# Kernel optimization log

Hardware: AMD Instinct MI355X
Metric: run time of the kernel (lower is better)

Reference implementation:

```python
import jax, jax.numpy as jnp
import numpy as np

# Config (matches init_kwargs)
B, S = 2, 2048            # 2 packed sequences of 2048 tokens (prefill)
HQ, HK, D = 32, 8, 128    # GQA: 32 query heads, 8 kv heads
G = HQ // HK              # group size 4
WINDOW = 1024             # sliding window
THETA = 10000.0


def setup_inputs() -> dict:
    key = jax.random.key(0)
    kq, kk, kv = jax.random.split(key, 3)
    n_tokens = B * S
    query = jax.random.normal(kq, (n_tokens, HQ * D), dtype=jnp.float32)
    key_t = jax.random.normal(kk, (n_tokens, HK * D), dtype=jnp.float32)
    value = jax.random.normal(kv, (n_tokens, HK * D), dtype=jnp.float32)
    # per-sequence positions restart at 0 for each packed sequence
    positions = jnp.tile(jnp.arange(S, dtype=jnp.int32), B)
    return {"query": query, "key": key_t, "value": value, "positions": positions}


def _rope(x, positions):
    # x: [B, S, H, D]; rotate-half (NeoX) RoPE
    half = D // 2
    inv_freq = 1.0 / (THETA ** (jnp.arange(0, half, dtype=jnp.float32) / half))
    ang = positions.astype(jnp.float32)[:, None] * inv_freq[None, :]   # [B*S, D/2]
    cos = jnp.cos(ang).reshape(B, S, 1, half)
    sin = jnp.sin(ang).reshape(B, S, 1, half)
    x1, x2 = x[..., :half], x[..., half:]
    return jnp.concatenate([x1 * cos - x2 * sin, x2 * cos + x1 * sin], axis=-1)


def reference(query, key, value, positions):
    q = query.reshape(B, S, HQ, D)
    k = key.reshape(B, S, HK, D)
    v = value.reshape(B, S, HK, D)
    q = _rope(q, positions)
    k = _rope(k, positions)
    # GQA: split q heads into [HK, G]
    qg = q.reshape(B, S, HK, G, D)
    scale = 1.0 / jnp.sqrt(jnp.float32(D))
    # scores: [B, HK, G, Sq, Skv]
    scores = jnp.einsum('bqhgd,bshd->bhgqs', qg, k) * scale
    i = jnp.arange(S)[:, None]
    j = jnp.arange(S)[None, :]
    # causal + sliding window: j <= i and i - j < WINDOW
    mask = (j <= i) & ((i - j) < WINDOW)
    scores = jnp.where(mask[None, None, None], scores, jnp.float32(-1e30))
    attn = jax.nn.softmax(scores, axis=-1)
    out = jnp.einsum('bhgqs,bshd->bqhgd', attn, v)   # [B, Sq, HK, G, D]
    return out.reshape(B * S, HQ * D)
```

## Files before the change

### kernel.cpp

```cpp
#include <hip/hip_runtime.h>
#include <stdint.h>

#define NB 2
#define NS 2048
#define NHK 8
#define ND 128
#define NWIN 1024

using bf16x8 = __bf16 __attribute__((ext_vector_type(8)));
using f32x4  = float  __attribute__((ext_vector_type(4)));
using f32x2  = float  __attribute__((ext_vector_type(2)));
using f32x8  = float  __attribute__((ext_vector_type(8)));
using u16x8  = unsigned short __attribute__((ext_vector_type(8)));
using u32x4  = unsigned int   __attribute__((ext_vector_type(4)));

#define L2_10K (13.287712379549449f / 64.0f)
#define MASKV (-3.0e38f)

static __device__ __forceinline__ float ex2(float x) {
  return __builtin_amdgcn_exp2f(x);
}

static __device__ __forceinline__ unsigned short f2bf(float x) {
  unsigned int u = __builtin_bit_cast(unsigned int, x);
  u += 0x7FFFu + ((u >> 16) & 1u);
  return (unsigned short)(u >> 16);
}

static __device__ __forceinline__ unsigned int cvtpk(float lo, float hi) {
  unsigned int r;
  asm("v_cvt_pk_bf16_f32 %0, %1, %2" : "=v"(r) : "v"(lo), "v"(hi));
  return r;
}

static __device__ __forceinline__ void gll16(const void* g, void* l) {
  __builtin_amdgcn_global_load_lds(
      (const __attribute__((address_space(1))) void*)g,
      (__attribute__((address_space(3))) void*)l, 16, 0, 0);
}

__global__ __launch_bounds__(64) void build_tab(float* __restrict__ tab) {
  const int p = blockIdx.x, f = threadIdx.x;
  float s, c;
  __sincosf((float)p * ex2(-(float)f * L2_10K), &s, &c);
  tab[(size_t)p * 128 + f] = c;
  tab[(size_t)p * 128 + 64 + f] = s;
}

__global__ __launch_bounds__(256) void prepass(
    const float* __restrict__ kin, const float* __restrict__ vin,
    const int* __restrict__ pos, const float* __restrict__ tab,
    unsigned short* __restrict__ kimg, unsigned short* __restrict__ vimg) {
  const int bid = blockIdx.x;
  const int ti = bid & 63, gidx = bid >> 6;
  const int hk = gidx & 7, b = gidx >> 3;
  const int t = threadIdx.x;

  unsigned short* kout = kimg + (size_t)bid * 4096;
#pragma unroll
  for (int uu = 0; uu < 2; ++uu) {
    const int u = t * 2 + uu;
    const int j = u >> 4;
    const int d0 = ((u & 15) << 3) ^ ((j & 7) << 3);
    const int tok = (b << 11) + (ti << 5) + j;
    const float* kp = kin + (size_t)tok * (NHK * ND) + hk * ND;
    f32x8 a = *(const f32x8*)(kp + d0);
    f32x8 p = *(const f32x8*)(kp + (d0 ^ 64));
    const float* tr = tab + (size_t)(pos[tok] & 2047) * 128 + (d0 & 63);
    f32x8 c8 = *(const f32x8*)tr;
    f32x8 s8 = *(const f32x8*)(tr + 64);
    u16x8 o;
#pragma unroll
    for (int i = 0; i < 8; ++i) {
      float val = (d0 < 64) ? (a[i] * c8[i] - p[i] * s8[i])
                            : (a[i] * c8[i] + p[i] * s8[i]);
      o[i] = f2bf(val);
    }
    *(u16x8*)(kout + (size_t)u * 8) = o;
  }

  unsigned short* vout = vimg + (size_t)bid * 4096;
  {
    const int d0 = (t >> 2) << 1;
    const int kp4 = t & 3;
    const int tok0 = (b << 11) + (ti << 5) + (kp4 << 3);
    const float* vp = vin + (size_t)tok0 * (NHK * ND) + hk * ND + d0;
    u16x8 lo, hi;
#pragma unroll
    for (int i = 0; i < 8; ++i) {
      f32x2 r = *(const f32x2*)(vp + (size_t)i * (NHK * ND));
      lo[i] = f2bf(r[0]);
      hi[i] = f2bf(r[1]);
    }
    const int sub = kp4 ^ ((d0 >> 1) & 3);
    *(u16x8*)(vout + d0 * 32 + sub * 8) = lo;
    *(u16x8*)(vout + (d0 + 1) * 32 + sub * 8) = hi;
  }
}

template <bool PRE>
__global__ __launch_bounds__(256, 3) void attn_fwd(
    const float* __restrict__ qin, const float* __restrict__ kin,
    const float* __restrict__ vin, const int* __restrict__ pos,
    const char* __restrict__ kimg, const char* __restrict__ vimg,
    float* __restrict__ out) {
  __shared__ __align__(16) char Kb[2][8192];
  __shared__ __align__(16) char Vb[2][8192];

  const int B = blockIdx.x;
  const int group = (B & 7) + ((B >> 9) << 3);
  const int qt = 63 - ((B >> 3) & 63);
  const int hk = group & 7, b = group >> 3;

  const int tid = threadIdx.x;
  const int w = tid >> 6, lane = tid & 63, h = lane >> 4, ln = lane & 15;
  const int g = w;
  const int q0b = qt << 5;
  int lo = q0b - (NWIN - 1);
  if (lo < 0) lo = 0;
  lo &= ~31;
  const int ti0 = lo >> 5;
  const int nt = (q0b >> 5) - ti0 + 1;

  const size_t gbase = (size_t)group * 64 * 8192;
  const char* kg = PRE ? kimg + gbase + (size_t)(w * 128 + lane) * 16 : nullptr;
  const char* vg = PRE ? vimg + gbase + (size_t)(w * 128 + lane) * 16 : nullptr;

  auto stage = [&](int cur, int ti) {
    if constexpr (PRE) {
      const char* ks = kg + (size_t)ti * 8192;
      const char* vs = vg + (size_t)ti * 8192;
      char* kd = &Kb[cur][w * 2048];
      char* vd = &Vb[cur][w * 2048];
      gll16(ks, kd);
      gll16(ks + 1024, kd + 1024);
      gll16(vs, vd);
      gll16(vs + 1024, vd + 1024);
    } else {
      const int j = tid >> 3;
      const int du = (tid & 7) << 4;
      const int tok = (b << 11) + (ti << 5) + j;
      const float* kp = kin + (size_t)tok * (NHK * ND) + hk * ND;
      const float pj = (float)pos[tok];
#pragma unroll
      for (int gq = 0; gq < 2; ++gq) {
        const int dd = du + gq * 8;
        f32x8 a = *(const f32x8*)(kp + dd);
        f32x8 p = *(const f32x8*)(kp + (dd ^ 64));
        u16x8 o;
#pragma unroll
        for (int i = 0; i < 8; ++i) {
          float s, c;
          __sincosf(pj * ex2(-(float)((dd & 63) + i) * L2_10K), &s, &c);
          float val = (dd < 64) ? (a[i] * c - p[i] * s) : (a[i] * c + p[i] * s);
          o[i] = f2bf(val);
        }
        *(u16x8*)(&Kb[cur][((j << 8) + (dd << 1)) ^ ((j & 7) << 4)]) = o;
      }
      const int d0 = (tid >> 2) << 1;
      const int kp4 = tid & 3;
      const float* vp = vin + (size_t)((b << 11) + (ti << 5) + (kp4 << 3)) * (NHK * ND) + hk * ND + d0;
      u16x8 lov, hiv;
#pragma unroll
      for (int i = 0; i < 8; ++i) {
        f32x2 r = *(const f32x2*)(vp + (size_t)i * (NHK * ND));
        lov[i] = f2bf(r[0]);
        hiv[i] = f2bf(r[1]);
      }
      const int sub = kp4 ^ ((d0 >> 1) & 3);
      unsigned short* vb16 = (unsigned short*)Vb[cur];
      *(u16x8*)(vb16 + d0 * 32 + sub * 8) = lov;
      *(u16x8*)(vb16 + (d0 + 1) * 32 + sub * 8) = hiv;
    }
  };

  stage(0, ti0);

  const float QSC = 0.08838834764831845f * 1.4426950408889634f;
  bf16x8 qfr[2][4];
#pragma unroll
  for (int hf = 0; hf < 2; ++hf) {
    const int qrow = q0b + hf * 16 + ln;
    const size_t tokq = (size_t)(b << 11) + qrow;
    const float* qp = qin + tokq * 4096 + (hk * 4 + g) * 128;
    const float posq = (float)pos[tokq];
    const int r0 = h << 3;
    const int r1 = 32 + (h << 3);
    f32x8 a0 = *(const f32x8*)(qp + r0);
    f32x8 a1 = *(const f32x8*)(qp + r1);
    f32x8 a2 = *(const f32x8*)(qp + r0 + 64);
    f32x8 a3 = *(const f32x8*)(qp + r1 + 64);
    u16x8 u0, u1, u2, u3;
#pragma unroll
    for (int i = 0; i < 8; ++i) {
      float c0, s0, c1, s1;
      __sincosf(posq * ex2(-(float)(r0 + i) * L2_10K), &s0, &c0);
      __sincosf(posq * ex2(-(float)(r1 + i) * L2_10K), &s1, &c1);
      u0[i] = f2bf((a0[i] * c0 - a2[i] * s0) * QSC);
      u1[i] = f2bf((a1[i] * c1 - a3[i] * s1) * QSC);
      u2[i] = f2bf((a2[i] * c0 + a0[i] * s0) * QSC);
      u3[i] = f2bf((a3[i] * c1 + a1[i] * s1) * QSC);
    }
    qfr[hf][0] = __builtin_bit_cast(bf16x8, u0);
    qfr[hf][1] = __builtin_bit_cast(bf16x8, u1);
    qfr[hf][2] = __builtin_bit_cast(bf16x8, u2);
    qfr[hf][3] = __builtin_bit_cast(bf16x8, u3);
  }

  f32x4 Oc[2][8] = {};
  float msh[2] = {-1e30f, -1e30f};
  float lsum[2] = {};
  const int sw = (ln & 7) << 4;
  const int vsub = (h ^ ((ln >> 1) & 3)) << 4;

  for (int t = 0; t < nt; ++t) {
    const int cur = t & 1;
    asm volatile("s_waitcnt vmcnt(0)" ::: "memory");
    __syncthreads();
    if (t + 1 < nt) stage(cur ^ 1, ti0 + t + 1);

    const int j0 = (ti0 + t) << 5;
    const char* KB = Kb[cur];

    f32x4 sT[2][2] = {};
    __builtin_amdgcn_s_setprio(1);
#pragma unroll
    for (int c = 0; c < 4; ++c) {
      const bf16x8 k0 = *(const bf16x8*)(
          KB + (((ln << 8) + (c << 6) + (h << 4)) ^ sw));
      const bf16x8 k1 = *(const bf16x8*)(
          KB + ((((16 + ln) << 8) + (c << 6) + (h << 4)) ^ sw));
      sT[0][0] = __builtin_amdgcn_mfma_f32_16x16x32_bf16(k0, qfr[0][c], sT[0][0], 0, 0, 0);
      sT[0][1] = __builtin_amdgcn_mfma_f32_16x16x32_bf16(k1, qfr[0][c], sT[0][1], 0, 0, 0);
      sT[1][0] = __builtin_amdgcn_mfma_f32_16x16x32_bf16(k0, qfr[1][c], sT[1][0], 0, 0, 0);
      sT[1][1] = __builtin_amdgcn_mfma_f32_16x16x32_bf16(k1, qfr[1][c], sT[1][1], 0, 0, 0);
    }
    __builtin_amdgcn_s_setprio(0);

    if ((j0 >= q0b) || (j0 < q0b - 992)) {
#pragma unroll
      for (int qh = 0; qh < 2; ++qh) {
        const int irow = q0b + qh * 16 + ln;
#pragma unroll
        for (int ki = 0; ki < 2; ++ki)
#pragma unroll
          for (int r = 0; r < 4; ++r) {
            const int j = j0 + ki * 16 + (h << 2) + r;
            if (!(j <= irow && irow - j < NWIN)) sT[qh][ki][r] = MASKV;
          }
      }
    }

    float pm[2];
#pragma unroll
    for (int qh = 0; qh < 2; ++qh) {
      const f32x4 s0 = sT[qh][0], s1 = sT[qh][1];
      pm[qh] = fmaxf(fmaxf(fmaxf(s0[0], s0[1]), fmaxf(s0[2], s0[3])),
                     fmaxf(fmaxf(s1[0], s1[1]), fmaxf(s1[2], s1[3])));
    }
    const float ov = fmaxf(pm[0] - msh[0], pm[1] - msh[1]);
    if (__any(ov > 8.0f)) {
#pragma unroll
      for (int qh = 0; qh < 2; ++qh) {
        float M = pm[qh];
        M = fmaxf(M, __shfl_xor(M, 16));
        M = fmaxf(M, __shfl_xor(M, 32));
        const float mn = fmaxf(msh[qh], M);
        const float co = ex2(msh[qh] - mn);
        msh[qh] = mn;
        lsum[qh] *= co;
        float coO[4];
#pragma unroll
        for (int r = 0; r < 4; ++r) coO[r] = __shfl(co, (h << 2) + r);
#pragma unroll
        for (int db = 0; db < 8; ++db)
#pragma unroll
          for (int r = 0; r < 4; ++r) Oc[qh][db][r] *= coO[r];
      }
    }

    bf16x8 pa[2];
#pragma unroll
    for (int qh = 0; qh < 2; ++qh) {
      float e[2][4];
#pragma unroll
      for (int ki = 0; ki < 2; ++ki)
#pragma unroll
        for (int r = 0; r < 4; ++r) e[ki][r] = ex2(sT[qh][ki][r] - msh[qh]);
      lsum[qh] += ((e[0][0] + e[0][1]) + (e[0][2] + e[0][3])) +
                  ((e[1][0] + e[1][1]) + (e[1][2] + e[1][3]));
      unsigned int A = cvtpk(e[0][0], e[0][1]);
      unsigned int Bk = cvtpk(e[0][2], e[0][3]);
      unsigned int C = cvtpk(e[1][0], e[1][1]);
      unsigned int D = cvtpk(e[1][2], e[1][3]);
      asm volatile("v_permlane32_swap_b32 %0, %1" : "+v"(A), "+v"(C));
      asm volatile("v_permlane16_swap_b32 %0, %1" : "+v"(A), "+v"(C));
      asm volatile("v_permlane32_swap_b32 %0, %1" : "+v"(Bk), "+v"(D));
      asm volatile("v_permlane16_swap_b32 %0, %1" : "+v"(Bk), "+v"(D));
      u32x4 pk4 = {A, Bk, C, D};
      pa[qh] = __builtin_bit_cast(bf16x8, pk4);
    }

    const char* VB = Vb[cur];
    __builtin_amdgcn_s_setprio(1);
#pragma unroll
    for (int db = 0; db < 8; ++db) {
      const bf16x8 vv = *(const bf16x8*)(VB + (db << 10) + (ln << 6) + vsub);
      Oc[0][db] = __builtin_amdgcn_mfma_f32_16x16x32_bf16(pa[0], vv, Oc[0][db], 0, 0, 0);
      Oc[1][db] = __builtin_amdgcn_mfma_f32_16x16x32_bf16(pa[1], vv, Oc[1][db], 0, 0, 0);
    }
    __builtin_amdgcn_s_setprio(0);
  }

#pragma unroll
  for (int qh = 0; qh < 2; ++qh) {
    float ls = lsum[qh];
    ls += __shfl_xor(ls, 16);
    ls += __shfl_xor(ls, 32);
#pragma unroll
    for (int r = 0; r < 4; ++r) {
      const float rl = 1.0f / __shfl(ls, (h << 2) + r);
      const int irow = q0b + qh * 16 + (h << 2) + r;
      float* op = out + ((size_t)(b << 11) + irow) * 4096 + (hk * 4 + g) * 128 + ln;
#pragma unroll
      for (int db = 0; db < 8; ++db) op[db * 16] = Oc[qh][db][r] * rl;
    }
  }
}

extern "C" void kernel_launch(void* const* d_in, const int* in_sizes, int n_in,
                              void* d_out, int out_size, void* d_ws, size_t ws_size,
                              hipStream_t stream) {
  const float* q = (const float*)d_in[0];
  const float* k = (const float*)d_in[1];
  const float* v = (const float*)d_in[2];
  const int* pos = (const int*)d_in[3];
  float* out = (float*)d_out;

  const size_t TAB = (size_t)2048 * 128 * 4;
  const size_t KIMG = (size_t)16 * 64 * 8192;
  const size_t need = TAB + 2 * KIMG;

  if (ws_size >= need) {
    float* tab = (float*)d_ws;
    char* kimg = (char*)d_ws + TAB;
    char* vimg = kimg + KIMG;
    build_tab<<<2048, 64, 0, stream>>>(tab);
    prepass<<<1024, 256, 0, stream>>>(k, v, pos, tab,
                                      (unsigned short*)kimg, (unsigned short*)vimg);
    attn_fwd<true><<<1024, 256, 0, stream>>>(q, k, v, pos, kimg, vimg, out);
  } else {
    attn_fwd<false><<<1024, 256, 0, stream>>>(q, k, v, pos, nullptr, nullptr, out);
  }
}
```

Baseline: 94.15 us.

## Software-pipeline PV MFMA one tile behind QK and use RoPE table for Q

Result: no change. 95.23 us (+1.2%).

```diff
diff --git a/kernel.cpp b/kernel.cpp
--- a/kernel.cpp
+++ b/kernel.cpp
@@ -38,6 +38,11 @@
       (const __attribute__((address_space(1))) void*)g,
       (__attribute__((address_space(3))) void*)l, 16, 0, 0);
 }
+
+#define MFMA16(a, b, c) __builtin_amdgcn_mfma_f32_16x16x32_bf16((a), (b), (c), 0, 0, 0)
+
+#define ROR(x, N) __builtin_bit_cast(float, __builtin_amdgcn_mov_dpp( \
+    __builtin_bit_cast(int, (x)), 0x120 + (N), 0xF, 0xF, false))
 
 __global__ __launch_bounds__(64) void build_tab(float* __restrict__ tab) {
   const int p = blockIdx.x, f = threadIdx.x;
@@ -103,9 +108,9 @@
     const float* __restrict__ qin, const float* __restrict__ kin,
     const float* __restrict__ vin, const int* __restrict__ pos,
     const char* __restrict__ kimg, const char* __restrict__ vimg,
-    float* __restrict__ out) {
+    const float* __restrict__ tab, float* __restrict__ out) {
   __shared__ __align__(16) char Kb[2][8192];
-  __shared__ __align__(16) char Vb[2][8192];
+  __shared__ __align__(16) char Vb[3][8192];
 
   const int B = blockIdx.x;
   const int group = (B & 7) + ((B >> 9) << 3);
@@ -126,16 +131,16 @@
   const char* kg = PRE ? kimg + gbase + (size_t)(w * 128 + lane) * 16 : nullptr;
   const char* vg = PRE ? vimg + gbase + (size_t)(w * 128 + lane) * 16 : nullptr;
 
-  auto stage = [&](int cur, int ti) {
+  auto stage = [&](int ks, int vs, int ti) {
     if constexpr (PRE) {
-      const char* ks = kg + (size_t)ti * 8192;
-      const char* vs = vg + (size_t)ti * 8192;
-      char* kd = &Kb[cur][w * 2048];
-      char* vd = &Vb[cur][w * 2048];
-      gll16(ks, kd);
-      gll16(ks + 1024, kd + 1024);
-      gll16(vs, vd);
-      gll16(vs + 1024, vd + 1024);
+      const char* ksrc = kg + (size_t)ti * 8192;
+      const char* vsrc = vg + (size_t)ti * 8192;
+      char* kd = &Kb[ks][w * 2048];
+      char* vd = &Vb[vs][w * 2048];
+      gll16(ksrc, kd);
+      gll16(ksrc + 1024, kd + 1024);
+      gll16(vsrc, vd);
+      gll16(vsrc + 1024, vd + 1024);
     } else {
       const int j = tid >> 3;
       const int du = (tid & 7) << 4;
@@ -155,7 +160,7 @@
           float val = (dd < 64) ? (a[i] * c - p[i] * s) : (a[i] * c + p[i] * s);
           o[i] = f2bf(val);
         }
-        *(u16x8*)(&Kb[cur][((j << 8) + (dd << 1)) ^ ((j & 7) << 4)]) = o;
+        *(u16x8*)(&Kb[ks][((j << 8) + (dd << 1)) ^ ((j & 7) << 4)]) = o;
       }
       const int d0 = (tid >> 2) << 1;
       const int kp4 = tid & 3;
@@ -168,13 +173,13 @@
         hiv[i] = f2bf(r[1]);
       }
       const int sub = kp4 ^ ((d0 >> 1) & 3);
-      unsigned short* vb16 = (unsigned short*)Vb[cur];
+      unsigned short* vb16 = (unsigned short*)Vb[vs];
       *(u16x8*)(vb16 + d0 * 32 + sub * 8) = lov;
       *(u16x8*)(vb16 + (d0 + 1) * 32 + sub * 8) = hiv;
     }
   };
 
-  stage(0, ti0);
+  stage(0, 0, ti0);
 
   const float QSC = 0.08838834764831845f * 1.4426950408889634f;
   bf16x8 qfr[2][4];
@@ -183,57 +188,75 @@
     const int qrow = q0b + hf * 16 + ln;
     const size_t tokq = (size_t)(b << 11) + qrow;
     const float* qp = qin + tokq * 4096 + (hk * 4 + g) * 128;
-    const float posq = (float)pos[tokq];
-    const int r0 = h << 3;
-    const int r1 = 32 + (h << 3);
-    f32x8 a0 = *(const f32x8*)(qp + r0);
-    f32x8 a1 = *(const f32x8*)(qp + r1);
-    f32x8 a2 = *(const f32x8*)(qp + r0 + 64);
-    f32x8 a3 = *(const f32x8*)(qp + r1 + 64);
-    u16x8 u0, u1, u2, u3;
-#pragma unroll
-    for (int i = 0; i < 8; ++i) {
-      float c0, s0, c1, s1;
-      __sincosf(posq * ex2(-(float)(r0 + i) * L2_10K), &s0, &c0);
-      __sincosf(posq * ex2(-(float)(r1 + i) * L2_10K), &s1, &c1);
-      u0[i] = f2bf((a0[i] * c0 - a2[i] * s0) * QSC);
-      u1[i] = f2bf((a1[i] * c1 - a3[i] * s1) * QSC);
-      u2[i] = f2bf((a2[i] * c0 + a0[i] * s0) * QSC);
-      u3[i] = f2bf((a3[i] * c1 + a1[i] * s1) * QSC);
-    }
-    qfr[hf][0] = __builtin_bit_cast(bf16x8, u0);
-    qfr[hf][1] = __builtin_bit_cast(bf16x8, u1);
-    qfr[hf][2] = __builtin_bit_cast(bf16x8, u2);
-    qfr[hf][3] = __builtin_bit_cast(bf16x8, u3);
+    const int posq = pos[tokq] & 2047;
+#pragma unroll
+    for (int pp = 0; pp < 2; ++pp) {
+      const int rr = (pp << 5) + (h << 3);
+      f32x8 lo8 = *(const f32x8*)(qp + rr);
+      f32x8 hi8 = *(const f32x8*)(qp + rr + 64);
+      f32x8 cc, ss;
+      if constexpr (PRE) {
+        const float* tp = tab + (size_t)posq * 128 + rr;
+        cc = *(const f32x8*)tp;
+        ss = *(const f32x8*)(tp + 64);
+      } else {
+        const float pf = (float)posq;
+#pragma unroll
+        for (int i = 0; i < 8; ++i) {
+          float s, c;
+          __sincosf(pf * ex2(-(float)(rr + i) * L2_10K), &s, &c);
+          cc[i] = c;
+          ss[i] = s;
+        }
+      }
+      u16x8 ulo, uhi;
+#pragma unroll
+      for (int i = 0; i < 8; ++i) {
+        ulo[i] = f2bf((lo8[i] * cc[i] - hi8[i] * ss[i]) * QSC);
+        uhi[i] = f2bf((hi8[i] * cc[i] + lo8[i] * ss[i]) * QSC);
+      }
+      qfr[hf][pp] = __builtin_bit_cast(bf16x8, ulo);
+      qfr[hf][2 + pp] = __builtin_bit_cast(bf16x8, uhi);
+    }
   }
 
   f32x4 Oc[2][8] = {};
   float msh[2] = {-1e30f, -1e30f};
   float lsum[2] = {};
+  bf16x8 pap0, pap1;
   const int sw = (ln & 7) << 4;
   const int vsub = (h ^ ((ln >> 1) & 3)) << 4;
+  int vsp = 2, vsc = 0, vsn = 1;
 
   for (int t = 0; t < nt; ++t) {
-    const int cur = t & 1;
     asm volatile("s_waitcnt vmcnt(0)" ::: "memory");
     __syncthreads();
-    if (t + 1 < nt) stage(cur ^ 1, ti0 + t + 1);
+    if (t + 1 < nt) stage((t + 1) & 1, vsn, ti0 + t + 1);
 
     const int j0 = (ti0 + t) << 5;
-    const char* KB = Kb[cur];
-
+    const char* KB = Kb[t & 1];
+    const char* VB = Vb[vsp];
+
+    __builtin_amdgcn_s_setprio(1);
+    if (t > 0) {
+#pragma unroll
+      for (int db = 0; db < 8; ++db) {
+        const bf16x8 vv = *(const bf16x8*)(VB + (db << 10) + (ln << 6) + vsub);
+        Oc[0][db] = MFMA16(pap0, vv, Oc[0][db]);
+        Oc[1][db] = MFMA16(pap1, vv, Oc[1][db]);
+      }
+    }
     f32x4 sT[2][2] = {};
-    __builtin_amdgcn_s_setprio(1);
 #pragma unroll
     for (int c = 0; c < 4; ++c) {
       const bf16x8 k0 = *(const bf16x8*)(
           KB + (((ln << 8) + (c << 6) + (h << 4)) ^ sw));
       const bf16x8 k1 = *(const bf16x8*)(
           KB + ((((16 + ln) << 8) + (c << 6) + (h << 4)) ^ sw));
-      sT[0][0] = __builtin_amdgcn_mfma_f32_16x16x32_bf16(k0, qfr[0][c], sT[0][0], 0, 0, 0);
-      sT[0][1] = __builtin_amdgcn_mfma_f32_16x16x32_bf16(k1, qfr[0][c], sT[0][1], 0, 0, 0);
-      sT[1][0] = __builtin_amdgcn_mfma_f32_16x16x32_bf16(k0, qfr[1][c], sT[1][0], 0, 0, 0);
-      sT[1][1] = __builtin_amdgcn_mfma_f32_16x16x32_bf16(k1, qfr[1][c], sT[1][1], 0, 0, 0);
+      sT[0][0] = MFMA16(k0, qfr[0][c], sT[0][0]);
+      sT[0][1] = MFMA16(k1, qfr[0][c], sT[0][1]);
+      sT[1][0] = MFMA16(k0, qfr[1][c], sT[1][0]);
+      sT[1][1] = MFMA16(k1, qfr[1][c], sT[1][1]);
     }
     __builtin_amdgcn_s_setprio(0);
 
@@ -278,38 +301,40 @@
           for (int r = 0; r < 4; ++r) Oc[qh][db][r] *= coO[r];
       }
     }
-
-    bf16x8 pa[2];
 #pragma unroll
     for (int qh = 0; qh < 2; ++qh) {
-      float e[2][4];
 #pragma unroll
       for (int ki = 0; ki < 2; ++ki)
 #pragma unroll
-        for (int r = 0; r < 4; ++r) e[ki][r] = ex2(sT[qh][ki][r] - msh[qh]);
-      lsum[qh] += ((e[0][0] + e[0][1]) + (e[0][2] + e[0][3])) +
-                  ((e[1][0] + e[1][1]) + (e[1][2] + e[1][3]));
-      unsigned int A = cvtpk(e[0][0], e[0][1]);
-      unsigned int Bk = cvtpk(e[0][2], e[0][3]);
-      unsigned int C = cvtpk(e[1][0], e[1][1]);
-      unsigned int D = cvtpk(e[1][2], e[1][3]);
+        for (int r = 0; r < 4; ++r)
+          sT[qh][ki][r] = ex2(sT[qh][ki][r] - msh[qh]);
+      lsum[qh] += ((sT[qh][0][0] + sT[qh][0][1]) + (sT[qh][0][2] + sT[qh][0][3])) +
+                  ((sT[qh][1][0] + sT[qh][1][1]) + (sT[qh][1][2] + sT[qh][1][3]));
+      unsigned int A = cvtpk(sT[qh][0][0], sT[qh][0][1]);
+      unsigned int Bk = cvtpk(sT[qh][0][2], sT[qh][0][3]);
+      unsigned int C = cvtpk(sT[qh][1][0], sT[qh][1][1]);
+      unsigned int D = cvtpk(sT[qh][1][2], sT[qh][1][3]);
       asm volatile("v_permlane32_swap_b32 %0, %1" : "+v"(A), "+v"(C));
       asm volatile("v_permlane16_swap_b32 %0, %1" : "+v"(A), "+v"(C));
       asm volatile("v_permlane32_swap_b32 %0, %1" : "+v"(Bk), "+v"(D));
       asm volatile("v_permlane16_swap_b32 %0, %1" : "+v"(Bk), "+v"(D));
       u32x4 pk4 = {A, Bk, C, D};
-      pa[qh] = __builtin_bit_cast(bf16x8, pk4);
-    }
-
-    const char* VB = Vb[cur];
-    __builtin_amdgcn_s_setprio(1);
+      if (qh == 0) pap0 = __builtin_bit_cast(bf16x8, pk4);
+      else         pap1 = __builtin_bit_cast(bf16x8, pk4);
+    }
+
+    const int tmp = vsp;
+    vsp = vsc; vsc = vsn; vsn = tmp;
+  }
+
+  {
+    const char* VB = Vb[vsp];
 #pragma unroll
     for (int db = 0; db < 8; ++db) {
       const bf16x8 vv = *(const bf16x8*)(VB + (db << 10) + (ln << 6) + vsub);
-      Oc[0][db] = __builtin_amdgcn_mfma_f32_16x16x32_bf16(pa[0], vv, Oc[0][db], 0, 0, 0);
-      Oc[1][db] = __builtin_amdgcn_mfma_f32_16x16x32_bf16(pa[1], vv, Oc[1][db], 0, 0, 0);
-    }
-    __builtin_amdgcn_s_setprio(0);
+      Oc[0][db] = MFMA16(pap0, vv, Oc[0][db]);
+      Oc[1][db] = MFMA16(pap1, vv, Oc[1][db]);
+    }
   }
 
 #pragma unroll
@@ -348,8 +373,8 @@
     build_tab<<<2048, 64, 0, stream>>>(tab);
     prepass<<<1024, 256, 0, stream>>>(k, v, pos, tab,
                                       (unsigned short*)kimg, (unsigned short*)vimg);
-    attn_fwd<true><<<1024, 256, 0, stream>>>(q, k, v, pos, kimg, vimg, out);
+    attn_fwd<true><<<1024, 256, 0, stream>>>(q, k, v, pos, kimg, vimg, tab, out);
   } else {
-    attn_fwd<false><<<1024, 256, 0, stream>>>(q, k, v, pos, nullptr, nullptr, out);
-  }
-}
+    attn_fwd<false><<<1024, 256, 0, stream>>>(q, k, v, pos, nullptr, nullptr, nullptr, out);
+  }
+}
```
